# Optimization experiments

Measured on AMD Instinct MI355X. Metric: run time of the kernel, lower is better.

The kernel has to match this reference:

```python
import jax, jax.numpy as jnp
import numpy as np

LR = 0.01        # memory update learning rate (init kwarg lr)
INIT_SCALE = 0.01
B, N, D = 8, 1024, 256


def setup_inputs() -> dict:
    key = jax.random.key(0)
    k1, k2, k3, k4, k5 = jax.random.split(key, 5)
    return {
        "sequence": jax.random.normal(k1, (B, N, D), dtype=jnp.float32),
        "targets": jax.random.normal(k2, (B, N, D), dtype=jnp.float32),
        "theta0": jax.random.normal(k3, (D, D), dtype=jnp.float32) * INIT_SCALE,
        "W_e": jax.random.normal(k4, (D, D), dtype=jnp.float32) * INIT_SCALE,
        "W_o": jax.random.normal(k5, (D, D), dtype=jnp.float32) * INIT_SCALE,
    }


def reference(sequence, targets, theta0, W_e, W_o):
    # process_sequence on (batch, n, d) with targets: theta is reset to theta0
    # for each batch element, then updated sequentially per token (delta rule).
    def step(theta, xt):
        x_t, tgt_t = xt                      # (d,), (d,)
        h = W_e @ x_t                        # encode: F.linear(x, W_e)
        pred = theta @ h                     # predict with current memory
        err = tgt_t - pred
        theta_new = theta + LR * jnp.outer(err, h)   # rank-1 fast-weight update
        out = W_o @ pred                     # output projection of PREDICTION
        return theta_new, out

    def per_batch(seq_b, tgt_b):             # (n, d), (n, d)
        _, outs = jax.lax.scan(step, theta0, (seq_b, tgt_b))
        return outs                          # (n, d)

    return jax.vmap(per_batch)(sequence, targets)   # (batch, n, d)
```

## Files before the change

kernel.cpp:

```cpp
#include <hip/hip_runtime.h>

#define LR_C 0.01f
#define NB 8
#define NTOK 1024
#define DD 256
#define CH 8
#define NCHUNK (NTOK / CH)

#define DPP_ADD(x, ctrl) \
    ((x) + __int_as_float(__builtin_amdgcn_update_dpp( \
        0, __float_as_int(x), (ctrl), 0xF, 0xF, true)))

#define REDUCE_ALL64(s) do { \
    s = DPP_ADD(s, 0xB1); \
    s = DPP_ADD(s, 0x4E); \
    s = DPP_ADD(s, 0x141); \
    s = DPP_ADD(s, 0x140); \
    s += __shfl_xor(s, 16, 64); \
    s += __shfl_xor(s, 32, 64); \
} while (0)

#define TBM 64
#define TBN 64
#define TBK 16

__global__ __launch_bounds__(256) void gemm_abt_kernel(
    const float* __restrict__ A, const float* __restrict__ B,
    float* __restrict__ C)
{
    __shared__ float As[TBK][TBM + 4];
    __shared__ float Bs[TBK][TBN + 4];
    const int t    = threadIdx.x;
    const int lrow = t >> 2, lk = (t & 3) * 4;
    const int tx   = t & 15, ty = t >> 4;

    const float* Ap = A + (size_t)(blockIdx.x * TBM + lrow) * DD + lk;
    const float* Bp = B + (size_t)(blockIdx.y * TBN + lrow) * DD + lk;

    float4 acc[4];
    #pragma unroll
    for (int i = 0; i < 4; ++i) acc[i] = make_float4(0.f, 0.f, 0.f, 0.f);

    float4 a0 = *reinterpret_cast<const float4*>(Ap);
    float4 b0 = *reinterpret_cast<const float4*>(Bp);

    for (int k0 = 0; k0 < DD; k0 += TBK) {
        __syncthreads();
        As[lk + 0][lrow] = a0.x; As[lk + 1][lrow] = a0.y;
        As[lk + 2][lrow] = a0.z; As[lk + 3][lrow] = a0.w;
        Bs[lk + 0][lrow] = b0.x; Bs[lk + 1][lrow] = b0.y;
        Bs[lk + 2][lrow] = b0.z; Bs[lk + 3][lrow] = b0.w;
        __syncthreads();
        if (k0 + TBK < DD) {
            a0 = *reinterpret_cast<const float4*>(Ap + k0 + TBK);
            b0 = *reinterpret_cast<const float4*>(Bp + k0 + TBK);
        }
        #pragma unroll
        for (int k = 0; k < TBK; ++k) {
            float4 av = *reinterpret_cast<const float4*>(&As[k][ty * 4]);
            float4 bv = *reinterpret_cast<const float4*>(&Bs[k][tx * 4]);
            acc[0].x = fmaf(av.x, bv.x, acc[0].x); acc[0].y = fmaf(av.x, bv.y, acc[0].y);
            acc[0].z = fmaf(av.x, bv.z, acc[0].z); acc[0].w = fmaf(av.x, bv.w, acc[0].w);
            acc[1].x = fmaf(av.y, bv.x, acc[1].x); acc[1].y = fmaf(av.y, bv.y, acc[1].y);
            acc[1].z = fmaf(av.y, bv.z, acc[1].z); acc[1].w = fmaf(av.y, bv.w, acc[1].w);
            acc[2].x = fmaf(av.z, bv.x, acc[2].x); acc[2].y = fmaf(av.z, bv.y, acc[2].y);
            acc[2].z = fmaf(av.z, bv.z, acc[2].z); acc[2].w = fmaf(av.z, bv.w, acc[2].w);
            acc[3].x = fmaf(av.w, bv.x, acc[3].x); acc[3].y = fmaf(av.w, bv.y, acc[3].y);
            acc[3].z = fmaf(av.w, bv.z, acc[3].z); acc[3].w = fmaf(av.w, bv.w, acc[3].w);
        }
    }
    #pragma unroll
    for (int i = 0; i < 4; ++i) {
        float* cp = C + (size_t)(blockIdx.x * TBM + ty * 4 + i) * DD
                      + blockIdx.y * TBN + tx * 4;
        *reinterpret_cast<float4*>(cp) = acc[i];
    }
}

__global__ __launch_bounds__(64) void gram_kernel(
    const float* __restrict__ H, float* __restrict__ Gram)
{
    const int blk  = blockIdx.x;
    const int lane = threadIdx.x;
    const float* Hc = H + (size_t)blk * CH * DD + lane * 4;

    float4 h[CH];
    #pragma unroll
    for (int i = 0; i < CH; ++i)
        h[i] = *reinterpret_cast<const float4*>(Hc + (size_t)i * DD);

    float sel = 0.f;
    #pragma unroll
    for (int i = 1; i < CH; ++i) {
        #pragma unroll
        for (int j = 0; j < i; ++j) {
            float s = h[j].x * h[i].x;
            s = fmaf(h[j].y, h[i].y, s);
            s = fmaf(h[j].z, h[i].z, s);
            s = fmaf(h[j].w, h[i].w, s);
            REDUCE_ALL64(s);
            const int idx = i * (i - 1) / 2 + j;
            sel = (lane == idx) ? s : sel;
        }
    }
    if (lane < 28) Gram[(size_t)blk * 32 + lane] = sel;
}

#define STEP(HC, TC, CC, HN, TN, CN, ch) do { \
    const int nc_ = ((ch) + 1 < NCHUNK) ? (ch) + 1 : NCHUNK - 1; \
    const float* hsrc_ = Hb + (size_t)nc_ * CH * DD; \
    const float* tsrc_ = Tb + (size_t)nc_ * CH * DD; \
    const float* gsrc_ = Gb + nc_ * 32; \
    _Pragma("unroll") \
    for (int i_ = 0; i_ < CH; ++i_) { \
        HN[i_] = *reinterpret_cast<const float4*>(hsrc_ + (size_t)i_ * DD); \
        TN[i_] = LR_C * tsrc_[(size_t)i_ * DD]; \
    } \
    _Pragma("unroll") \
    for (int q_ = 0; q_ < 28; ++q_) CN[q_] = gsrc_[q_]; \
    float a_[CH]; \
    _Pragma("unroll") \
    for (int i_ = 0; i_ < CH; ++i_) { \
        float s_ = HC[i_].x * th.x; \
        s_ = fmaf(HC[i_].y, th.y, s_); \
        s_ = fmaf(HC[i_].z, th.z, s_); \
        s_ = fmaf(HC[i_].w, th.w, s_); \
        REDUCE_ALL64(s_); \
        a_[i_] = s_; \
    } \
    float e_[CH], p_[CH]; \
    _Pragma("unroll") \
    for (int i_ = 0; i_ < CH; ++i_) { \
        float pv_ = a_[i_]; \
        _Pragma("unroll") \
        for (int j_ = 0; j_ < i_; ++j_) \
            pv_ = fmaf(e_[j_], CC[i_ * (i_ - 1) / 2 + j_], pv_); \
        p_[i_] = pv_; \
        e_[i_] = fmaf(-LR_C, pv_, TC[i_]); \
    } \
    _Pragma("unroll") \
    for (int j_ = 0; j_ < CH; ++j_) { \
        th.x = fmaf(e_[j_], HC[j_].x, th.x); \
        th.y = fmaf(e_[j_], HC[j_].y, th.y); \
        th.z = fmaf(e_[j_], HC[j_].z, th.z); \
        th.w = fmaf(e_[j_], HC[j_].w, th.w); \
    } \
    float sel_ = p_[0]; \
    _Pragma("unroll") \
    for (int i_ = 1; i_ < CH; ++i_) sel_ = (lane == i_) ? p_[i_] : sel_; \
    if (lane < CH) Pb[(size_t)((ch) * CH + lane) * DD] = sel_; \
} while (0)

__global__ __launch_bounds__(64) void theta_scan_kernel(
    const float* __restrict__ H, const float* __restrict__ Tgt,
    const float* __restrict__ theta0, const float* __restrict__ Gram,
    float* __restrict__ Pred)
{
    const int blk  = blockIdx.x;
    const int b    = blk >> 8;
    const int row  = blk & 255;
    const int lane = threadIdx.x;

    float4 th = *reinterpret_cast<const float4*>(
        theta0 + (size_t)row * DD + lane * 4);

    const float* Hb = H    + (size_t)b * NTOK * DD + lane * 4;
    const float* Tb = Tgt  + (size_t)b * NTOK * DD + row;
    const float* Gb = Gram + (size_t)b * NCHUNK * 32;
    float*       Pb = Pred + (size_t)b * NTOK * DD + row;

    float4 hA[CH]; float tA[CH], cA[28];
    float4 hB[CH]; float tB[CH], cB[28];

    #pragma unroll
    for (int i = 0; i < CH; ++i) {
        hA[i] = *reinterpret_cast<const float4*>(Hb + (size_t)i * DD);
        tA[i] = LR_C * Tb[(size_t)i * DD];
    }
    #pragma unroll
    for (int q = 0; q < 28; ++q) cA[q] = Gb[q];

    for (int ch = 0; ch < NCHUNK; ch += 2) {
        STEP(hA, tA, cA, hB, tB, cB, ch);
        STEP(hB, tB, cB, hA, tA, cA, ch + 1);
    }
}

extern "C" void kernel_launch(void* const* d_in, const int* in_sizes, int n_in,
                              void* d_out, int out_size, void* d_ws, size_t ws_size,
                              hipStream_t stream) {
    const float* seq    = (const float*)d_in[0];
    const float* tgt    = (const float*)d_in[1];
    const float* theta0 = (const float*)d_in[2];
    const float* W_e    = (const float*)d_in[3];
    const float* W_o    = (const float*)d_in[4];
    float* out = (float*)d_out;

    float* Hbuf = (float*)d_ws;
    float* Pbuf = Hbuf + (size_t)NB * NTOK * DD;
    float* Cbuf = out;

    dim3 ggrid(NB * NTOK / TBM, DD / TBN);

    gemm_abt_kernel<<<ggrid, 256, 0, stream>>>(seq, W_e, Hbuf);
    gram_kernel<<<NB * NCHUNK, 64, 0, stream>>>(Hbuf, Cbuf);
    theta_scan_kernel<<<NB * 256, 64, 0, stream>>>(Hbuf, tgt, theta0, Cbuf, Pbuf);
    gemm_abt_kernel<<<ggrid, 256, 0, stream>>>(Pbuf, W_o, out);
}
```

Baseline: 223.6 us.

## Store predictions transposed, vectorize Gram loads, interleave batch scan blocks

The scan kernel now writes predictions in a transposed layout (batch, row, token), so each block's 8 per-chunk outputs land contiguously instead of DD apart. A new GEMM variant reads that transposed layout for the output projection. Gram coefficients are loaded as float4 with a scheduling barrier. Scan blocks are interleaved across batches so concurrent blocks share H chunks, and the Gram kernel splits its reductions over two waves. The extra transposed GEMM A-loads and the larger grid reshaping may shift cache behavior.

```diff
diff --git a/kernel.cpp b/kernel.cpp
--- a/kernel.cpp
+++ b/kernel.cpp
@@ -77,12 +77,73 @@
     }
 }
 
-__global__ __launch_bounds__(64) void gram_kernel(
+__global__ __launch_bounds__(256) void gemm_pt_kernel(
+    const float* __restrict__ PT, const float* __restrict__ B,
+    float* __restrict__ C)
+{
+    __shared__ float As[TBK][TBM + 4];
+    __shared__ float Bs[TBK][TBN + 4];
+    const int t  = threadIdx.x;
+    const int mb = blockIdx.x;
+    const int b  = mb >> 4;
+    const int t0 = (mb & 15) * TBM;
+    const int bn = blockIdx.y;
+
+    const int akrow = t >> 4, amcol = (t & 15) * 4;
+    const int brow  = t >> 2, bk    = (t & 3) * 4;
+    const int tx    = t & 15, ty    = t >> 4;
+
+    const float* Ap = PT + (size_t)b * DD * NTOK + (size_t)akrow * NTOK + t0 + amcol;
+    const float* Bp = B + (size_t)(bn * TBN + brow) * DD + bk;
+
+    float4 acc[4];
+    #pragma unroll
+    for (int i = 0; i < 4; ++i) acc[i] = make_float4(0.f, 0.f, 0.f, 0.f);
+
+    float4 a0 = *reinterpret_cast<const float4*>(Ap);
+    float4 b0 = *reinterpret_cast<const float4*>(Bp);
+
+    for (int k0 = 0; k0 < DD; k0 += TBK) {
+        __syncthreads();
+        *reinterpret_cast<float4*>(&As[akrow][amcol]) = a0;
+        Bs[bk + 0][brow] = b0.x; Bs[bk + 1][brow] = b0.y;
+        Bs[bk + 2][brow] = b0.z; Bs[bk + 3][brow] = b0.w;
+        __syncthreads();
+        if (k0 + TBK < DD) {
+            a0 = *reinterpret_cast<const float4*>(Ap + (size_t)(k0 + TBK) * NTOK);
+            b0 = *reinterpret_cast<const float4*>(Bp + k0 + TBK);
+        }
+        #pragma unroll
+        for (int k = 0; k < TBK; ++k) {
+            float4 av = *reinterpret_cast<const float4*>(&As[k][ty * 4]);
+            float4 bv = *reinterpret_cast<const float4*>(&Bs[k][tx * 4]);
+            acc[0].x = fmaf(av.x, bv.x, acc[0].x); acc[0].y = fmaf(av.x, bv.y, acc[0].y);
+            acc[0].z = fmaf(av.x, bv.z, acc[0].z); acc[0].w = fmaf(av.x, bv.w, acc[0].w);
+            acc[1].x = fmaf(av.y, bv.x, acc[1].x); acc[1].y = fmaf(av.y, bv.y, acc[1].y);
+            acc[1].z = fmaf(av.y, bv.z, acc[1].z); acc[1].w = fmaf(av.y, bv.w, acc[1].w);
+            acc[2].x = fmaf(av.z, bv.x, acc[2].x); acc[2].y = fmaf(av.z, bv.y, acc[2].y);
+            acc[2].z = fmaf(av.z, bv.z, acc[2].z); acc[2].w = fmaf(av.z, bv.w, acc[2].w);
+            acc[3].x = fmaf(av.w, bv.x, acc[3].x); acc[3].y = fmaf(av.w, bv.y, acc[3].y);
+            acc[3].z = fmaf(av.w, bv.z, acc[3].z); acc[3].w = fmaf(av.w, bv.w, acc[3].w);
+        }
+    }
+    #pragma unroll
+    for (int i = 0; i < 4; ++i) {
+        float* cp = C + (size_t)(b * NTOK + t0 + ty * 4 + i) * DD
+                      + bn * TBN + tx * 4;
+        *reinterpret_cast<float4*>(cp) = acc[i];
+    }
+}
+
+__global__ __launch_bounds__(128) void gram_kernel(
     const float* __restrict__ H, float* __restrict__ Gram)
 {
     const int blk  = blockIdx.x;
-    const int lane = threadIdx.x;
-    const float* Hc = H + (size_t)blk * CH * DD + lane * 4;
+    const int b    = blk & 7;
+    const int chk  = blk >> 3;
+    const int w    = threadIdx.x >> 6;
+    const int lane = threadIdx.x & 63;
+    const float* Hc = H + ((size_t)b * NTOK + (size_t)chk * CH) * DD + lane * 4;
 
     float4 h[CH];
     #pragma unroll
@@ -94,30 +155,36 @@
     for (int i = 1; i < CH; ++i) {
         #pragma unroll
         for (int j = 0; j < i; ++j) {
-            float s = h[j].x * h[i].x;
-            s = fmaf(h[j].y, h[i].y, s);
-            s = fmaf(h[j].z, h[i].z, s);
-            s = fmaf(h[j].w, h[i].w, s);
-            REDUCE_ALL64(s);
             const int idx = i * (i - 1) / 2 + j;
-            sel = (lane == idx) ? s : sel;
-        }
-    }
-    if (lane < 28) Gram[(size_t)blk * 32 + lane] = sel;
-}
+            if ((idx & 1) == w) {
+                float s = h[j].x * h[i].x;
+                s = fmaf(h[j].y, h[i].y, s);
+                s = fmaf(h[j].z, h[i].z, s);
+                s = fmaf(h[j].w, h[i].w, s);
+                REDUCE_ALL64(s);
+                sel = (lane == idx) ? s : sel;
+            }
+        }
+    }
+    if (lane < 28 && (lane & 1) == w)
+        Gram[((size_t)b * NCHUNK + chk) * 32 + lane] = sel;
+}
+
+#define GC(Cb, q) (((const float*)&(Cb)[0])[(q)])
 
 #define STEP(HC, TC, CC, HN, TN, CN, ch) do { \
     const int nc_ = ((ch) + 1 < NCHUNK) ? (ch) + 1 : NCHUNK - 1; \
     const float* hsrc_ = Hb + (size_t)nc_ * CH * DD; \
     const float* tsrc_ = Tb + (size_t)nc_ * CH * DD; \
-    const float* gsrc_ = Gb + nc_ * 32; \
+    const float4* gsrc_ = reinterpret_cast<const float4*>(Gb + nc_ * 32); \
     _Pragma("unroll") \
     for (int i_ = 0; i_ < CH; ++i_) { \
         HN[i_] = *reinterpret_cast<const float4*>(hsrc_ + (size_t)i_ * DD); \
         TN[i_] = LR_C * tsrc_[(size_t)i_ * DD]; \
     } \
     _Pragma("unroll") \
-    for (int q_ = 0; q_ < 28; ++q_) CN[q_] = gsrc_[q_]; \
+    for (int q_ = 0; q_ < 7; ++q_) CN[q_] = gsrc_[q_]; \
+    __builtin_amdgcn_sched_barrier(0); \
     float a_[CH]; \
     _Pragma("unroll") \
     for (int i_ = 0; i_ < CH; ++i_) { \
@@ -134,7 +201,7 @@
         float pv_ = a_[i_]; \
         _Pragma("unroll") \
         for (int j_ = 0; j_ < i_; ++j_) \
-            pv_ = fmaf(e_[j_], CC[i_ * (i_ - 1) / 2 + j_], pv_); \
+            pv_ = fmaf(e_[j_], GC(CC, i_ * (i_ - 1) / 2 + j_), pv_); \
         p_[i_] = pv_; \
         e_[i_] = fmaf(-LR_C, pv_, TC[i_]); \
     } \
@@ -148,17 +215,17 @@
     float sel_ = p_[0]; \
     _Pragma("unroll") \
     for (int i_ = 1; i_ < CH; ++i_) sel_ = (lane == i_) ? p_[i_] : sel_; \
-    if (lane < CH) Pb[(size_t)((ch) * CH + lane) * DD] = sel_; \
+    if (lane < CH) Pb[(ch) * CH + lane] = sel_; \
 } while (0)
 
-__global__ __launch_bounds__(64) void theta_scan_kernel(
+__global__ __launch_bounds__(64, 2) void theta_scan_kernel(
     const float* __restrict__ H, const float* __restrict__ Tgt,
     const float* __restrict__ theta0, const float* __restrict__ Gram,
-    float* __restrict__ Pred)
+    float* __restrict__ PT)
 {
     const int blk  = blockIdx.x;
-    const int b    = blk >> 8;
-    const int row  = blk & 255;
+    const int b    = blk & 7;
+    const int row  = blk >> 3;
     const int lane = threadIdx.x;
 
     float4 th = *reinterpret_cast<const float4*>(
@@ -167,10 +234,10 @@
     const float* Hb = H    + (size_t)b * NTOK * DD + lane * 4;
     const float* Tb = Tgt  + (size_t)b * NTOK * DD + row;
     const float* Gb = Gram + (size_t)b * NCHUNK * 32;
-    float*       Pb = Pred + (size_t)b * NTOK * DD + row;
-
-    float4 hA[CH]; float tA[CH], cA[28];
-    float4 hB[CH]; float tB[CH], cB[28];
+    float*       Pb = PT   + ((size_t)b * DD + row) * NTOK;
+
+    float4 hA[CH]; float tA[CH]; float4 cA[7];
+    float4 hB[CH]; float tB[CH]; float4 cB[7];
 
     #pragma unroll
     for (int i = 0; i < CH; ++i) {
@@ -178,7 +245,8 @@
         tA[i] = LR_C * Tb[(size_t)i * DD];
     }
     #pragma unroll
-    for (int q = 0; q < 28; ++q) cA[q] = Gb[q];
+    for (int q = 0; q < 7; ++q)
+        cA[q] = reinterpret_cast<const float4*>(Gb)[q];
 
     for (int ch = 0; ch < NCHUNK; ch += 2) {
         STEP(hA, tA, cA, hB, tB, cB, ch);
@@ -196,14 +264,14 @@
     const float* W_o    = (const float*)d_in[4];
     float* out = (float*)d_out;
 
-    float* Hbuf = (float*)d_ws;
-    float* Pbuf = Hbuf + (size_t)NB * NTOK * DD;
+    float* Hbuf  = (float*)d_ws;
+    float* PTbuf = Hbuf + (size_t)NB * NTOK * DD;
     float* Cbuf = out;
 
     dim3 ggrid(NB * NTOK / TBM, DD / TBN);
 
     gemm_abt_kernel<<<ggrid, 256, 0, stream>>>(seq, W_e, Hbuf);
-    gram_kernel<<<NB * NCHUNK, 64, 0, stream>>>(Hbuf, Cbuf);
-    theta_scan_kernel<<<NB * 256, 64, 0, stream>>>(Hbuf, tgt, theta0, Cbuf, Pbuf);
-    gemm_abt_kernel<<<ggrid, 256, 0, stream>>>(Pbuf, W_o, out);
-}
+    gram_kernel<<<NB * NCHUNK, 128, 0, stream>>>(Hbuf, Cbuf);
+    theta_scan_kernel<<<NB * 256, 64, 0, stream>>>(Hbuf, tgt, theta0, Cbuf, PTbuf);
+    gemm_pt_kernel<<<ggrid, 256, 0, stream>>>(PTbuf, W_o, out);
+}
```

Result: faster. 213.9 us (-4.3%).
